# Optimization experiments

Hardware: AMD Instinct MI355X
Metric: run time of the kernel (lower is better)

The kernel has to match this reference:

```python
import jax, jax.numpy as jnp
import numpy as np

N_NODES = 20000


def setup_inputs() -> dict:
    key = jax.random.key(0)
    ks = jax.random.split(key, 6)
    d = 512
    E = 640000
    x = jax.random.normal(ks[0], (N_NODES, d), dtype=jnp.float32)
    edge_index = jax.random.randint(ks[1], (2, E), 0, N_NODES, dtype=jnp.int64)
    s = 1.0 / np.sqrt(d)
    W1 = jax.random.uniform(ks[2], (d, d), jnp.float32, -s, s)
    b1 = jax.random.uniform(ks[3], (d,), jnp.float32, -s, s)
    W2 = jax.random.uniform(ks[4], (d, d), jnp.float32, -s, s)
    b2 = jax.random.uniform(ks[5], (d,), jnp.float32, -s, s)
    return {"x": x, "edge_index": edge_index, "W1": W1, "b1": b1, "W2": W2, "b2": b2}


def reference(x, edge_index, W1, b1, W2, b2):
    eps = 0.0
    src, dst = edge_index[0], edge_index[1]
    # scatter-add neighbor aggregation: sum_{j in N(i)} x_j
    agg = jax.ops.segment_sum(x[src], dst, num_segments=N_NODES)  # [N, d]
    h = (1.0 + eps) * x + agg
    # MLP: Linear -> ReLU -> Linear
    h = jax.nn.relu(h @ W1 + b1)
    out = h @ W2 + b2
    return out
```

## Files before the change

kernel.cpp:

```cpp
#include <hip/hip_runtime.h>
#include <hip/hip_bf16.h>

typedef __attribute__((ext_vector_type(8))) short s16x8;
typedef __attribute__((ext_vector_type(4))) float f32x4;
typedef __attribute__((ext_vector_type(2))) float pf2;

#define D_FEAT 512
#define SLICES 8
#define SLICE_D 64
#define ROWS 80

__device__ __forceinline__ unsigned short f2bf(float f) {
  __hip_bfloat16 h = __float2bfloat16(f);
  return *reinterpret_cast<unsigned short*>(&h);
}

__device__ __forceinline__ float bitsf(unsigned int u) {
  union { unsigned int i; float f; } c;
  c.i = u;
  return c.f;
}

__device__ __forceinline__ void async16(void* lds, const void* g) {
  __builtin_amdgcn_global_load_lds(
      (const __attribute__((address_space(1))) void*)g,
      (__attribute__((address_space(3))) void*)lds, 16, 0, 0);
}


__global__ __launch_bounds__(256) void zero_k(int4* __restrict__ p, int n16) {
  int i = blockIdx.x * 256 + threadIdx.x;
  if (i < n16) p[i] = make_int4(0, 0, 0, 0);
}


__global__ __launch_bounds__(256) void hx_k(const int* __restrict__ dst, int E,
                                            int* __restrict__ deg,
                                            const float* __restrict__ x,
                                            unsigned short* __restrict__ xs, int n8, int hb,
                                            int Nn) {
  int bid = blockIdx.x;
  if (bid < hb) {
    int i = bid * 256 + threadIdx.x;
    if (i < E) atomicAdd(&deg[dst[i]], 1);
  } else {
    int i = (bid - hb) * 256 + threadIdx.x;
    if (i < n8) {
      int n = i >> 6;
      int c = i & 63;
      int s = c >> 3;
      int off = (c & 7);
      const float4* p = (const float4*)x + (size_t)i * 2;
      float4 u = p[0], v = p[1];
      s16x8 r;
      r[0] = (short)f2bf(u.x); r[1] = (short)f2bf(u.y);
      r[2] = (short)f2bf(u.z); r[3] = (short)f2bf(u.w);
      r[4] = (short)f2bf(v.x); r[5] = (short)f2bf(v.y);
      r[6] = (short)f2bf(v.z); r[7] = (short)f2bf(v.w);
      ((s16x8*)xs)[((size_t)s * Nn + n) * 8 + off] = r;
    }
  }
}


__global__ __launch_bounds__(1024) void scanw_k(const int* __restrict__ deg,
                                                int* __restrict__ rowstart,
                                                unsigned short* __restrict__ nodeord, int n,
                                                const float* __restrict__ W1,
                                                const float* __restrict__ W2,
                                                unsigned short* __restrict__ W1t,
                                                unsigned short* __restrict__ W2t) {
  if (blockIdx.x < 128) {
    __shared__ float tile[64][65];
    int t = blockIdx.x;
    const float* W = W1;
    unsigned short* Wt = W1t;
    if (t >= 64) { t -= 64; W = W2; Wt = W2t; }
    int tr = (t >> 3) * 64;
    int tc = (t & 7) * 64;
    int tid = threadIdx.x;
    int c4 = (tid & 15) * 4, r = tid >> 4;
    float4 vv = *(const float4*)&W[(size_t)(tr + r) * 512 + tc + c4];
    tile[r][c4] = vv.x; tile[r][c4 + 1] = vv.y; tile[r][c4 + 2] = vv.z; tile[r][c4 + 3] = vv.w;
    __syncthreads();
    int nn = tid >> 4;
    int k0 = (tid & 15) * 4;
    ushort4 o;
    o.x = f2bf(tile[k0 + 0][nn]);
    o.y = f2bf(tile[k0 + 1][nn]);
    o.z = f2bf(tile[k0 + 2][nn]);
    o.w = f2bf(tile[k0 + 3][nn]);
    *(ushort4*)&Wt[(size_t)(tc + nn) * 512 + tr + k0] = o;
    return;
  }
  __shared__ int wsum[16];
  __shared__ int carry_s;
  __shared__ int hist[65];
  int tid = threadIdx.x;
  int lane = tid & 63, wid = tid >> 6;
  if (tid == 0) carry_s = 0;
  __syncthreads();
  for (int t0 = 0; t0 < n; t0 += 4096) {
    int base = t0 + tid * 4;
    int e0, e1, e2, e3;
    if (base + 3 < n) {
      int4 v4 = *(const int4*)&deg[base];
      e0 = v4.x; e1 = v4.y; e2 = v4.z; e3 = v4.w;
    } else {
      e0 = (base + 0 < n) ? deg[base + 0] : 0;
      e1 = (base + 1 < n) ? deg[base + 1] : 0;
      e2 = (base + 2 < n) ? deg[base + 2] : 0;
      e3 = (base + 3 < n) ? deg[base + 3] : 0;
    }
    int lsum = e0 + e1 + e2 + e3;
    int s = lsum;
#pragma unroll
    for (int off = 1; off < 64; off <<= 1) {
      int t = __shfl_up(s, off);
      if (lane >= off) s += t;
    }
    if (lane == 63) wsum[wid] = s;
    __syncthreads();
    if (wid == 0) {
      int ws = (lane < 16) ? wsum[lane] : 0;
#pragma unroll
      for (int off = 1; off < 16; off <<= 1) {
        int t = __shfl_up(ws, off);
        if (lane >= off) ws += t;
      }
      if (lane < 16) wsum[lane] = ws;
    }
    __syncthreads();
    int carry = carry_s;
    int wbase = (wid > 0) ? wsum[wid - 1] : 0;
    int pre = carry + wbase + (s - lsum);
    if (base + 0 < n) rowstart[base + 0] = pre;
    if (base + 1 < n) rowstart[base + 1] = pre + e0;
    if (base + 2 < n) rowstart[base + 2] = pre + e0 + e1;
    if (base + 3 < n) rowstart[base + 3] = pre + e0 + e1 + e2;
    int total = wsum[15];
    __syncthreads();
    if (tid == 0) carry_s = carry + total;
    __syncthreads();
  }
  if (tid == 0) rowstart[n] = carry_s;
  if (tid < 65) hist[tid] = 0;
  __syncthreads();
  for (int i = tid; i < n; i += 1024) atomicAdd(&hist[min(deg[i], 64)], 1);
  __syncthreads();
  if (tid == 0) {
    int run = 0;
    for (int b = 0; b < 65; ++b) { int c = hist[b]; hist[b] = run; run += c; }
  }
  __syncthreads();
  for (int i = tid; i < n; i += 1024) {
    int b = min(deg[i], 64);
    int pos = atomicAdd(&hist[b], 1);
    nodeord[pos] = (unsigned short)i;
  }
}

__global__ void fill_k(const int* __restrict__ src, const int* __restrict__ dst, int E,
                       const int* __restrict__ rowstart, int* __restrict__ cursor,
                       unsigned short* __restrict__ ep16) {
  int i = blockIdx.x * 256 + threadIdx.x;
  if (i < E) {
    int d = dst[i];
    int pos = atomicAdd(&cursor[d], 1);
    ep16[rowstart[d] + pos] = (unsigned short)src[i];
  }
}


__global__ __launch_bounds__(256, 6) void agg_k(const unsigned short* __restrict__ xs,
                                                const int* __restrict__ rowstart,
                                                const unsigned short* __restrict__ ep16,
                                                const unsigned short* __restrict__ nodeord,
                                                unsigned short* __restrict__ h, int Nn) {
  int slice = blockIdx.x & 7;
  int nb = blockIdx.x >> 3;
  int wid = threadIdx.x >> 6, lane = threadIdx.x & 63;
  int g = lane >> 3, sub = lane & 7;
  int slot = (nb * 4 + wid) * 8 + g;
  int node = nodeord[slot];
  int beg = rowstart[node];
  int deg = rowstart[node + 1] - beg;
  int degm1 = max(deg - 1, 0);
  int dm = deg;
  dm = max(dm, __shfl_xor(dm, 8));
  dm = max(dm, __shfl_xor(dm, 16));
  dm = max(dm, __shfl_xor(dm, 32));
  const unsigned short* ep = ep16 + beg;
  const s16x8* sb = (const s16x8*)xs + (size_t)slice * Nn * 8;
  s16x8 own = sb[node * 8 + sub];
  pf2 acc[4];
#pragma unroll
  for (int q = 0; q < 4; ++q) {
    unsigned int d = (unsigned int)((const int*)&own)[q];
    acc[q].x = bitsf(d << 16);
    acc[q].y = bitsf(d & 0xffff0000u);
  }
  for (int t = 0; t < dm; t += 8) {
    s16x8 v[8];
    float m[8];
#pragma unroll
    for (int b = 0; b < 8; ++b) {
      int tt = t + b;
      int e = ep[min(tt, degm1)];
      m[b] = (tt < deg) ? 1.f : 0.f;
      v[b] = sb[e * 8 + sub];
    }
#pragma unroll
    for (int b = 0; b < 8; ++b) {
#pragma unroll
      for (int q = 0; q < 4; ++q) {
        unsigned int d = (unsigned int)((const int*)&v[b])[q];
        pf2 p;
        p.x = bitsf(d << 16);
        p.y = bitsf(d & 0xffff0000u);
        acc[q] += m[b] * p;
      }
    }
  }
  s16x8 r;
#pragma unroll
  for (int q = 0; q < 4; ++q) {
    r[q * 2 + 0] = (short)f2bf(acc[q].x);
    r[q * 2 + 1] = (short)f2bf(acc[q].y);
  }
  __builtin_nontemporal_store(r, (s16x8*)(h + (size_t)node * D_FEAT + slice * SLICE_D + sub * 8));
}


__global__ __launch_bounds__(1024, 1) void mlp_k(const unsigned short* __restrict__ A,
                                                 const unsigned short* __restrict__ W1t,
                                                 const unsigned short* __restrict__ W2t,
                                                 const float* __restrict__ b1,
                                                 const float* __restrict__ b2,
                                                 float* __restrict__ out, int M) {
  __shared__ unsigned short As[2][ROWS * 32];
  __shared__ unsigned short Bs[2][512 * 32];
  __shared__ unsigned short c1s[ROWS * 512];
  int tm = blockIdx.x;
  int tid = threadIdx.x;
  int wave = tid >> 6, lane = tid & 63;
  int lr = lane & 15, lh = lane >> 4;
  bool aw = tid < 320;

  auto ldschunk = [](int row, int c) {
    int p = row >> 1;
    return p * 8 + (((((row & 1) << 2) | c)) ^ (p & 7));
  };

  auto stage_b = [&](const unsigned short* Bt, int pb, int k0) {
#pragma unroll
    for (int ii = 0; ii < 2; ++ii) {
      int cb = ii * 1024 + tid;
      int p = cb >> 3;
      int s2 = (cb & 7) ^ (p & 7);
      int row = p * 2 + (s2 >> 2);
      int c = s2 & 3;
      async16(&Bs[pb][(size_t)(ii * 1024 + wave * 64) * 8], Bt + (size_t)row * 512 + k0 + c * 8);
    }
  };
  auto stage_a = [&](int pb, int k0) {
    if (aw) {
      int cb = tid;
      int p = cb >> 3;
      int s2 = (cb & 7) ^ (p & 7);
      int row = p * 2 + (s2 >> 2);
      int c = s2 & 3;
      int ga = min(tm * ROWS + row, M - 1);
      async16(&As[pb][(size_t)(wave * 64) * 8], A + (size_t)ga * 512 + k0 + c * 8);
    }
  };

  f32x4 zero = {0.f, 0.f, 0.f, 0.f};
  f32x4 acc[5][2];
#pragma unroll
  for (int rt = 0; rt < 5; ++rt)
#pragma unroll
    for (int ct = 0; ct < 2; ++ct) acc[rt][ct] = zero;

  stage_b(W1t, 0, 0);
  stage_a(0, 0);
#pragma unroll
  for (int t = 0; t < 16; ++t) {
    int pb = t & 1;
    if (t < 15) { stage_b(W1t, pb ^ 1, (t + 1) * 32); stage_a(pb ^ 1, (t + 1) * 32); }
    if (t < 15) {
      if (aw) asm volatile("s_waitcnt vmcnt(3)" ::: "memory");
      else    asm volatile("s_waitcnt vmcnt(2)" ::: "memory");
    } else {
      asm volatile("s_waitcnt vmcnt(0)" ::: "memory");
    }
    __builtin_amdgcn_s_barrier();
    s16x8 av[5], bv[2];
#pragma unroll
    for (int rt = 0; rt < 5; ++rt)
      av[rt] = *(const s16x8*)&As[pb][ldschunk(rt * 16 + lr, lh) * 8];
#pragma unroll
    for (int ct = 0; ct < 2; ++ct)
      bv[ct] = *(const s16x8*)&Bs[pb][ldschunk(wave * 32 + ct * 16 + lr, lh) * 8];
#pragma unroll
    for (int rt = 0; rt < 5; ++rt)
#pragma unroll
      for (int ct = 0; ct < 2; ++ct)
        acc[rt][ct] = __builtin_amdgcn_mfma_f32_16x16x32_bf16(av[rt], bv[ct], acc[rt][ct], 0, 0, 0);
    __builtin_amdgcn_s_barrier();
  }

  stage_b(W2t, 0, 0);

#pragma unroll
  for (int ct = 0; ct < 2; ++ct) {
    int col = wave * 32 + ct * 16 + lr;
    float bval = b1[col];
    int chunk = col >> 3;
#pragma unroll
    for (int rt = 0; rt < 5; ++rt) {
#pragma unroll
      for (int j = 0; j < 4; ++j) {
        int row = rt * 16 + lh * 4 + j;
        float v = fmaxf(acc[rt][ct][j] + bval, 0.f);
        c1s[row * 512 + ((chunk ^ (row & 7)) * 8) + (col & 7)] = f2bf(v);
      }
    }
  }
  __syncthreads();

#pragma unroll
  for (int rt = 0; rt < 5; ++rt)
#pragma unroll
    for (int ct = 0; ct < 2; ++ct) acc[rt][ct] = zero;

#pragma unroll
  for (int t = 0; t < 16; ++t) {
    int pb = t & 1;
    if (t < 15) stage_b(W2t, pb ^ 1, (t + 1) * 32);
    if (t < 15) asm volatile("s_waitcnt vmcnt(2)" ::: "memory");
    else        asm volatile("s_waitcnt vmcnt(0)" ::: "memory");
    __builtin_amdgcn_s_barrier();
    s16x8 av[5], bv[2];
#pragma unroll
    for (int rt = 0; rt < 5; ++rt) {
      int row = rt * 16 + lr;
      av[rt] = *(const s16x8*)&c1s[row * 512 + (((t * 4 + lh) ^ (row & 7)) * 8)];
    }
#pragma unroll
    for (int ct = 0; ct < 2; ++ct)
      bv[ct] = *(const s16x8*)&Bs[pb][ldschunk(wave * 32 + ct * 16 + lr, lh) * 8];
#pragma unroll
    for (int rt = 0; rt < 5; ++rt)
#pragma unroll
      for (int ct = 0; ct < 2; ++ct)
        acc[rt][ct] = __builtin_amdgcn_mfma_f32_16x16x32_bf16(av[rt], bv[ct], acc[rt][ct], 0, 0, 0);
    __builtin_amdgcn_s_barrier();
  }

#pragma unroll
  for (int ct = 0; ct < 2; ++ct) {
    int col = wave * 32 + ct * 16 + lr;
    float bval = b2[col];
#pragma unroll
    for (int rt = 0; rt < 5; ++rt) {
#pragma unroll
      for (int j = 0; j < 4; ++j) {
        int row = tm * ROWS + rt * 16 + lh * 4 + j;
        if (row < M)
          __builtin_nontemporal_store(acc[rt][ct][j] + bval, &out[(size_t)row * 512 + col]);
      }
    }
  }
}


extern "C" void kernel_launch(void* const* d_in, const int* in_sizes, int n_in,
                              void* d_out, int out_size, void* d_ws, size_t ws_size,
                              hipStream_t stream) {
  const float* x = (const float*)d_in[0];
  const int* ei = (const int*)d_in[1];
  const float* W1 = (const float*)d_in[2];
  const float* b1 = (const float*)d_in[3];
  const float* W2 = (const float*)d_in[4];
  const float* b2 = (const float*)d_in[5];
  const int N = in_sizes[0] / D_FEAT;
  const int E = in_sizes[1] / 2;
  const int* src = ei;
  const int* dst = ei + E;

  char* w = (char*)d_ws;
  auto alloc = [&](size_t bytes) {
    void* p = (void*)w;
    w += (bytes + 255) & ~(size_t)255;
    return p;
  };
  unsigned short* ep16 = (unsigned short*)alloc((size_t)E * 2 + 256);
  int* deg = (int*)alloc((size_t)N * 4);
  int* cursor = (int*)alloc((size_t)N * 4);
  int* rowstart = (int*)alloc((size_t)(N + 1) * 4);
  unsigned short* nodeord = (unsigned short*)alloc((size_t)N * 2);
  unsigned short* W1t = (unsigned short*)alloc((size_t)512 * 512 * 2);
  unsigned short* W2t = (unsigned short*)alloc((size_t)512 * 512 * 2);
  unsigned short* h = (unsigned short*)alloc((size_t)N * 512 * 2);
  unsigned short* xs = (unsigned short*)d_out + (size_t)N * D_FEAT;

  size_t zbytes = (size_t)((char*)cursor - (char*)deg) + (size_t)N * 4;
  int zn16 = (int)(zbytes / 16);
  zero_k<<<(zn16 + 255) / 256, 256, 0, stream>>>((int4*)deg, zn16);
  int hb = (E + 255) / 256;
  int n8 = N * D_FEAT / 8;
  int xbk = (n8 + 255) / 256;
  hx_k<<<hb + xbk, 256, 0, stream>>>(dst, E, deg, x, xs, n8, hb, N);
  scanw_k<<<129, 1024, 0, stream>>>(deg, rowstart, nodeord, N, W1, W2, W1t, W2t);
  fill_k<<<hb, 256, 0, stream>>>(src, dst, E, rowstart, cursor, ep16);
  agg_k<<<8 * (N / 32), 256, 0, stream>>>(xs, rowstart, ep16, nodeord, h, N);
  int mt = (N + ROWS - 1) / ROWS;
  mlp_k<<<mt, 1024, 0, stream>>>(h, W1t, W2t, b1, b2, (float*)d_out, N);
}
```

Baseline: 172.5 us.

## Move x conversion into scan kernel, vectorize edge passes, shrink aggregation unroll

The fp32-to-bf16 sliced conversion of x moves from the degree-count kernel into extra blocks of the scan/weight-transpose kernel, so it overlaps with the single-block scan instead of the atomic histogram. The degree and fill kernels now process four edges per thread using int4 loads. The aggregation kernel's gather unroll drops from 8 to 4 and its occupancy hint rises from 6 to 8 blocks, trading memory-level parallelism per wave for more resident waves. The converted x must be finished before agg_k, which holds because agg_k is launched after scanw_k.

```diff
diff --git a/kernel.cpp b/kernel.cpp
--- a/kernel.cpp
+++ b/kernel.cpp
@@ -35,30 +35,16 @@
 
 
 __global__ __launch_bounds__(256) void hx_k(const int* __restrict__ dst, int E,
-                                            int* __restrict__ deg,
-                                            const float* __restrict__ x,
-                                            unsigned short* __restrict__ xs, int n8, int hb,
-                                            int Nn) {
-  int bid = blockIdx.x;
-  if (bid < hb) {
-    int i = bid * 256 + threadIdx.x;
-    if (i < E) atomicAdd(&deg[dst[i]], 1);
+                                            int* __restrict__ deg) {
+  int i4 = (blockIdx.x * 256 + threadIdx.x) * 4;
+  if (i4 + 3 < E) {
+    int4 d4 = *(const int4*)&dst[i4];
+    atomicAdd(&deg[d4.x], 1);
+    atomicAdd(&deg[d4.y], 1);
+    atomicAdd(&deg[d4.z], 1);
+    atomicAdd(&deg[d4.w], 1);
   } else {
-    int i = (bid - hb) * 256 + threadIdx.x;
-    if (i < n8) {
-      int n = i >> 6;
-      int c = i & 63;
-      int s = c >> 3;
-      int off = (c & 7);
-      const float4* p = (const float4*)x + (size_t)i * 2;
-      float4 u = p[0], v = p[1];
-      s16x8 r;
-      r[0] = (short)f2bf(u.x); r[1] = (short)f2bf(u.y);
-      r[2] = (short)f2bf(u.z); r[3] = (short)f2bf(u.w);
-      r[4] = (short)f2bf(v.x); r[5] = (short)f2bf(v.y);
-      r[6] = (short)f2bf(v.z); r[7] = (short)f2bf(v.w);
-      ((s16x8*)xs)[((size_t)s * Nn + n) * 8 + off] = r;
-    }
+    for (int i = i4; i < E; ++i) atomicAdd(&deg[dst[i]], 1);
   }
 }
 
@@ -69,7 +55,9 @@
                                                 const float* __restrict__ W1,
                                                 const float* __restrict__ W2,
                                                 unsigned short* __restrict__ W1t,
-                                                unsigned short* __restrict__ W2t) {
+                                                unsigned short* __restrict__ W2t,
+                                                const float* __restrict__ x,
+                                                unsigned short* __restrict__ xs, int n8) {
   if (blockIdx.x < 128) {
     __shared__ float tile[64][65];
     int t = blockIdx.x;
@@ -93,6 +81,24 @@
     *(ushort4*)&Wt[(size_t)(tc + nn) * 512 + tr + k0] = o;
     return;
   }
+  if (blockIdx.x > 128) {
+    int i = (blockIdx.x - 129) * 1024 + threadIdx.x;
+    if (i < n8) {
+      int nd = i >> 6;
+      int c = i & 63;
+      int s = c >> 3;
+      int off = c & 7;
+      const float4* p = (const float4*)x + (size_t)i * 2;
+      float4 u = p[0], v = p[1];
+      s16x8 r;
+      r[0] = (short)f2bf(u.x); r[1] = (short)f2bf(u.y);
+      r[2] = (short)f2bf(u.z); r[3] = (short)f2bf(u.w);
+      r[4] = (short)f2bf(v.x); r[5] = (short)f2bf(v.y);
+      r[6] = (short)f2bf(v.z); r[7] = (short)f2bf(v.w);
+      ((s16x8*)xs)[((size_t)s * n + nd) * 8 + off] = r;
+    }
+    return;
+  }
   __shared__ int wsum[16];
   __shared__ int carry_s;
   __shared__ int hist[65];
@@ -160,19 +166,31 @@
   }
 }
 
-__global__ void fill_k(const int* __restrict__ src, const int* __restrict__ dst, int E,
-                       const int* __restrict__ rowstart, int* __restrict__ cursor,
-                       unsigned short* __restrict__ ep16) {
-  int i = blockIdx.x * 256 + threadIdx.x;
-  if (i < E) {
-    int d = dst[i];
-    int pos = atomicAdd(&cursor[d], 1);
-    ep16[rowstart[d] + pos] = (unsigned short)src[i];
-  }
-}
-
-
-__global__ __launch_bounds__(256, 6) void agg_k(const unsigned short* __restrict__ xs,
+
+__global__ __launch_bounds__(256) void fill_k(const int* __restrict__ src,
+                                              const int* __restrict__ dst, int E,
+                                              const int* __restrict__ rowstart,
+                                              int* __restrict__ cursor,
+                                              unsigned short* __restrict__ ep16) {
+  int i4 = (blockIdx.x * 256 + threadIdx.x) * 4;
+  if (i4 + 3 < E) {
+    int4 d4 = *(const int4*)&dst[i4];
+    int4 s4 = *(const int4*)&src[i4];
+    int p0 = atomicAdd(&cursor[d4.x], 1); ep16[rowstart[d4.x] + p0] = (unsigned short)s4.x;
+    int p1 = atomicAdd(&cursor[d4.y], 1); ep16[rowstart[d4.y] + p1] = (unsigned short)s4.y;
+    int p2 = atomicAdd(&cursor[d4.z], 1); ep16[rowstart[d4.z] + p2] = (unsigned short)s4.z;
+    int p3 = atomicAdd(&cursor[d4.w], 1); ep16[rowstart[d4.w] + p3] = (unsigned short)s4.w;
+  } else {
+    for (int i = i4; i < E; ++i) {
+      int d = dst[i];
+      int pos = atomicAdd(&cursor[d], 1);
+      ep16[rowstart[d] + pos] = (unsigned short)src[i];
+    }
+  }
+}
+
+
+__global__ __launch_bounds__(256, 8) void agg_k(const unsigned short* __restrict__ xs,
                                                 const int* __restrict__ rowstart,
                                                 const unsigned short* __restrict__ ep16,
                                                 const unsigned short* __restrict__ nodeord,
@@ -200,18 +218,18 @@
     acc[q].x = bitsf(d << 16);
     acc[q].y = bitsf(d & 0xffff0000u);
   }
-  for (int t = 0; t < dm; t += 8) {
-    s16x8 v[8];
-    float m[8];
-#pragma unroll
-    for (int b = 0; b < 8; ++b) {
+  for (int t = 0; t < dm; t += 4) {
+    s16x8 v[4];
+    float m[4];
+#pragma unroll
+    for (int b = 0; b < 4; ++b) {
       int tt = t + b;
       int e = ep[min(tt, degm1)];
       m[b] = (tt < deg) ? 1.f : 0.f;
       v[b] = sb[e * 8 + sub];
     }
 #pragma unroll
-    for (int b = 0; b < 8; ++b) {
+    for (int b = 0; b < 4; ++b) {
 #pragma unroll
       for (int q = 0; q < 4; ++q) {
         unsigned int d = (unsigned int)((const int*)&v[b])[q];
@@ -408,12 +426,13 @@
   size_t zbytes = (size_t)((char*)cursor - (char*)deg) + (size_t)N * 4;
   int zn16 = (int)(zbytes / 16);
   zero_k<<<(zn16 + 255) / 256, 256, 0, stream>>>((int4*)deg, zn16);
-  int hb = (E + 255) / 256;
+  int hb4 = (E / 4 + 255) / 256;
+  hx_k<<<hb4, 256, 0, stream>>>(dst, E, deg);
   int n8 = N * D_FEAT / 8;
-  int xbk = (n8 + 255) / 256;
-  hx_k<<<hb + xbk, 256, 0, stream>>>(dst, E, deg, x, xs, n8, hb, N);
-  scanw_k<<<129, 1024, 0, stream>>>(deg, rowstart, nodeord, N, W1, W2, W1t, W2t);
-  fill_k<<<hb, 256, 0, stream>>>(src, dst, E, rowstart, cursor, ep16);
+  int xbk = (n8 + 1023) / 1024;
+  scanw_k<<<129 + xbk, 1024, 0, stream>>>(deg, rowstart, nodeord, N, W1, W2, W1t, W2t,
+                                          x, xs, n8);
+  fill_k<<<hb4, 256, 0, stream>>>(src, dst, E, rowstart, cursor, ep16);
   agg_k<<<8 * (N / 32), 256, 0, stream>>>(xs, rowstart, ep16, nodeord, h, N);
   int mt = (N + ROWS - 1) / ROWS;
   mlp_k<<<mt, 1024, 0, stream>>>(h, W1t, W2t, b1, b2, (float*)d_out, N);
```

Result: no change. 173.0 us (+0.3%).
